# Performance work log

Measured on AMD Instinct MI355X. Metric: run time of the kernel, lower is better.

## Reference

```python
import jax, jax.numpy as jnp
import numpy as np

B, S, HID = 1, 2048, 4096
NH, NKV, D = 32, 8, 128
SCALE = D ** -0.5


def _rope_tables(seq_len, head_dim, base=10000.0):
    inv_freq = 1.0 / (base ** (jnp.arange(0, head_dim, 2, dtype=jnp.float32) / head_dim))
    freqs = jnp.arange(seq_len, dtype=jnp.float32)[:, None] * inv_freq[None, :]  # [S, D/2]
    emb = jnp.concatenate([freqs, freqs], axis=-1)  # [S, D]
    return jnp.cos(emb), jnp.sin(emb)


def _rotate_half(x):
    half = x.shape[-1] // 2
    return jnp.concatenate([-x[..., half:], x[..., :half]], axis=-1)


def setup_inputs() -> dict:
    key = jax.random.key(0)
    ks = jax.random.split(key, 5)
    hidden = jax.random.normal(ks[0], (B, S, HID), dtype=jnp.float32)
    cos, sin = _rope_tables(S, D)
    # additive causal mask: 0 on/below diagonal, large negative above
    neg = jnp.full((S, S), -1e9, dtype=jnp.float32)
    causal_mask = jnp.triu(neg, k=1)[None, None]  # [1,1,S,S]
    std_in = HID ** -0.5
    Wq = jax.random.normal(ks[1], (HID, NH * D), dtype=jnp.float32) * std_in
    Wk = jax.random.normal(ks[2], (HID, NKV * D), dtype=jnp.float32) * std_in
    Wv = jax.random.normal(ks[3], (HID, NKV * D), dtype=jnp.float32) * std_in
    Wo = jax.random.normal(ks[4], (NH * D, HID), dtype=jnp.float32) * ((NH * D) ** -0.5)
    return {"hidden": hidden, "cos": cos, "sin": sin, "causal_mask": causal_mask,
            "Wq": Wq, "Wk": Wk, "Wv": Wv, "Wo": Wo}


def reference(hidden, cos, sin, causal_mask, Wq, Wk, Wv, Wo):
    b, s, _ = hidden.shape
    q = (hidden @ Wq).reshape(b, s, NH, D).transpose(0, 2, 1, 3)    # [B,H,S,D]
    k = (hidden @ Wk).reshape(b, s, NKV, D).transpose(0, 2, 1, 3)   # [B,Hkv,S,D]
    v = (hidden @ Wv).reshape(b, s, NKV, D).transpose(0, 2, 1, 3)
    c = cos[None, None]  # [1,1,S,D]
    sn = sin[None, None]
    q = q * c + _rotate_half(q) * sn
    k = k * c + _rotate_half(k) * sn
    group = NH // NKV
    if group > 1:
        k = jnp.repeat(k, group, axis=1)  # [B,H,S,D]
        v = jnp.repeat(v, group, axis=1)
    scores = jnp.einsum('bhsd,bhtd->bhst', q, k) * SCALE + causal_mask
    attn = jax.nn.softmax(scores.astype(jnp.float32), axis=-1).astype(v.dtype)
    ctx = jnp.einsum('bhst,bhtd->bhsd', attn, v)
    ctx = ctx.transpose(0, 2, 1, 3).reshape(b, s, NH * D)
    return ctx @ Wo
```

## Files before the change

kernel.cpp:

```cpp
#include <hip/hip_runtime.h>
#include <hip/hip_bf16.h>
#include <cstdint>
#include <cstddef>

typedef __attribute__((ext_vector_type(8))) short bf16x8;
typedef __attribute__((ext_vector_type(4))) float f32x4;
typedef __attribute__((ext_vector_type(4))) unsigned int u32x4;

__device__ __forceinline__ unsigned short f2bf(float f) {
  __hip_bfloat16 h = __float2bfloat16(f);
  return *reinterpret_cast<unsigned short*>(&h);
}
__device__ __forceinline__ float bf2f(unsigned short u) {
  __hip_bfloat16 h = *reinterpret_cast<__hip_bfloat16*>(&u);
  return __bfloat162float(h);
}

typedef const __attribute__((address_space(1))) void gas_void;
typedef __attribute__((address_space(3))) void las_void;
__device__ __forceinline__ void gload_lds16(const void* g, void* l) {
  __builtin_amdgcn_global_load_lds((gas_void*)g, (las_void*)l, 16, 0, 0);
}

template <int N>
__device__ __forceinline__ void waitcnt_vm() {
  asm volatile("s_waitcnt vmcnt(%0)" :: "i"(N) : "memory");
}

#define S_LEN 2048
#define HID 4096
#define NH 32
#define NKV 8
#define HD 128
#define NQKV 6144
static const float ATT_SCALE = 0.08838834764831845f;


__global__ void cvt_f32_bf16_kernel(const float* __restrict__ src,
                                    short* __restrict__ dst, int n) {
  int i = (blockIdx.x * 256 + threadIdx.x) * 8;
  if (i >= n) return;
  f32x4 a = *(const f32x4*)(src + i);
  f32x4 b = *(const f32x4*)(src + i + 4);
  unsigned short t[8];
#pragma unroll
  for (int k = 0; k < 4; ++k) { t[k] = f2bf(a[k]); t[4 + k] = f2bf(b[k]); }
  *(u32x4*)(dst + i) = *(const u32x4*)t;
}

__global__ void transpose_cvt_kernel(const float* __restrict__ src,
                                     short* __restrict__ dst, int K, int N) {
  __shared__ float tile[64][33];
  const int kb = blockIdx.x * 64, nb = blockIdx.y * 32;
  const int t = threadIdx.x;
  {
    int kr = t >> 3, c4 = (t & 7) * 4;
#pragma unroll
    for (int i = 0; i < 2; ++i) {
      int k = kr + i * 32;
      f32x4 v = *(const f32x4*)(src + (size_t)(kb + k) * N + nb + c4);
      tile[k][c4] = v[0]; tile[k][c4 + 1] = v[1];
      tile[k][c4 + 2] = v[2]; tile[k][c4 + 3] = v[3];
    }
  }
  __syncthreads();
  int n = t >> 3, k0 = (t & 7) * 8;
  unsigned short o[8];
#pragma unroll
  for (int i = 0; i < 8; ++i) o[i] = f2bf(tile[k0 + i][n]);
  *(u32x4*)(dst + (size_t)(nb + n) * K + kb + k0) = *(const u32x4*)o;
}


#define READ_A(MHL) { \
    const short* As_ = lds + (kt & 1) * BUF; \
    _Pragma("unroll") for (int m = 0; m < MHALF; ++m) \
    _Pragma("unroll") for (int kk = 0; kk < 2; ++kk) { \
      int row = (MHL) * (BM / 2) + wr * MSTEP + m * 16 + r; \
      int c = kk * 4 + g; \
      af[m][kk] = *(const bf16x8*)(As_ + row * 64 + ((c ^ (row & 7)) * 8)); \
    } }
#define READ_B(NHL) { \
    const short* Bs_ = lds + (kt & 1) * BUF + BM * 64; \
    _Pragma("unroll") for (int n = 0; n < NHALF; ++n) \
    _Pragma("unroll") for (int kk = 0; kk < 2; ++kk) { \
      int row = (NHL) * (BN / 2) + wc * NSTEP + n * 16 + r; \
      int c = kk * 4 + g; \
      bf[n][kk] = *(const bf16x8*)(Bs_ + row * 64 + ((c ^ (row & 7)) * 8)); \
    } }
#define MFMA_QUAD(MHL, NHL) { \
    __builtin_amdgcn_s_setprio(1); \
    _Pragma("unroll") for (int m = 0; m < MHALF; ++m) \
    _Pragma("unroll") for (int n = 0; n < NHALF; ++n) \
    _Pragma("unroll") for (int kk = 0; kk < 2; ++kk) \
      acc[(MHL)*MHALF + m][(NHL)*NHALF + n] = __builtin_amdgcn_mfma_f32_16x16x32_bf16( \
          af[m][kk], bf[n][kk], acc[(MHL)*MHALF + m][(NHL)*NHALF + n], 0, 0, 0); \
    __builtin_amdgcn_s_setprio(0); }

template <int MODE, int BM, int BN, int WM, int WN>
__global__ __launch_bounds__(WM * WN * 64, 2) void gemm8p_kernel(
    const short* __restrict__ A, const short* __restrict__ Bt,
    int M, int N, int K,
    float* __restrict__ Cf, short* __restrict__ qb_,
    short* __restrict__ kb_, short* __restrict__ vb_) {
  constexpr int NT = WM * WN * 64;
  constexpr int M_FR = BM / (WM * 16);
  constexpr int N_FR = BN / (WN * 16);
  constexpr int MHALF = M_FR / 2;
  constexpr int NHALF = N_FR / 2;
  constexpr int MSTEP = BM / (2 * WM);
  constexpr int NSTEP = BN / (2 * WN);
  constexpr int LA = (BM / 2) * 8 / NT;
  constexpr int LB = (BN / 2) * 8 / NT;
  constexpr int BUF = (BM + BN) * 64;

  __shared__ short lds[2 * BUF];

  const int tid = threadIdx.x, wid = tid >> 6, lane = tid & 63;
  const int wr = wid / WN, wc = wid % WN;
  const int r = lane & 15, g = lane >> 4;
  const int brow = blockIdx.y * BM, bcol = blockIdx.x * BN;
  const int T = K >> 6;

  f32x4 acc[M_FR][N_FR] = {};
  bf16x8 af[MHALF][2], bf[NHALF][2];

  auto stage_rgn = [&](int kt, int rgn) {
    short* buf = lds + (kt & 1) * BUF;
    if (rgn == 0 || rgn == 3) {
      const int mh = (rgn == 3);
      short* dst = buf + mh * (BM / 2) * 64;
      const short* src = A + (size_t)(brow + mh * (BM / 2)) * K + kt * 64;
#pragma unroll
      for (int i = 0; i < LA; ++i) {
        int slot = i * NT + tid;
        int row = slot >> 3, c2 = slot & 7;
        gload_lds16(src + (size_t)row * K + ((c2 ^ (row & 7)) * 8), dst + slot * 8);
      }
    } else {
      const int nh = (rgn == 2);
      short* dst = buf + BM * 64 + nh * (BN / 2) * 64;
      const short* src = Bt + (size_t)(bcol + nh * (BN / 2)) * K + kt * 64;
#pragma unroll
      for (int i = 0; i < LB; ++i) {
        int slot = i * NT + tid;
        int row = slot >> 3, c2 = slot & 7;
        gload_lds16(src + (size_t)row * K + ((c2 ^ (row & 7)) * 8), dst + slot * 8);
      }
    }
  };

  stage_rgn(0, 0); stage_rgn(0, 1); stage_rgn(0, 2); stage_rgn(0, 3);

  for (int kt = 0; kt < T; ++kt) {
    const bool nl = (kt + 1 < T);
    waitcnt_vm<LA + LB>();
    __builtin_amdgcn_s_barrier();
    __builtin_amdgcn_sched_barrier(0);
    READ_A(0); READ_B(0);
    if (nl) stage_rgn(kt + 1, 0);
    MFMA_QUAD(0, 0);
    if (nl) { waitcnt_vm<2 * LA>(); } else { waitcnt_vm<LA>(); }
    __builtin_amdgcn_s_barrier();
    __builtin_amdgcn_sched_barrier(0);
    READ_B(1);
    if (nl) stage_rgn(kt + 1, 1);
    MFMA_QUAD(0, 1);
    if (nl) { waitcnt_vm<LA + LB>(); } else { waitcnt_vm<0>(); }
    __builtin_amdgcn_s_barrier();
    __builtin_amdgcn_sched_barrier(0);
    READ_A(1);
    if (nl) stage_rgn(kt + 1, 2);
    MFMA_QUAD(1, 1);
    READ_B(0);
    if (nl) stage_rgn(kt + 1, 3);
    MFMA_QUAD(1, 0);
  }

  if (MODE == 0) {
#pragma unroll
    for (int fm = 0; fm < M_FR; ++fm)
#pragma unroll
      for (int fn = 0; fn < N_FR; ++fn)
#pragma unroll
        for (int j = 0; j < 4; ++j) {
          int row = brow + (fm / MHALF) * (BM / 2) + wr * MSTEP + (fm % MHALF) * 16 + g * 4 + j;
          int col = bcol + (fn / NHALF) * (BN / 2) + wc * NSTEP + (fn % NHALF) * 16 + r;
          Cf[(size_t)row * N + col] = acc[fm][fn][j];
        }
  } else {
#pragma unroll
    for (int fn = 0; fn < N_FR; ++fn) {
      const int cb = bcol + (fn / NHALF) * (BN / 2) + wc * NSTEP + (fn % NHALF) * 16;
      if (cb < 4096) {
        unsigned short* dst = (unsigned short*)qb_ + (size_t)(cb >> 7) * S_LEN * HD;
        const int d0 = cb & 127;
#pragma unroll
        for (int fm = 0; fm < M_FR; ++fm)
#pragma unroll
          for (int j = 0; j < 4; ++j) {
            int row = brow + (fm / MHALF) * (BM / 2) + wr * MSTEP + (fm % MHALF) * 16 + g * 4 + j;
            dst[(size_t)row * HD + d0 + r] = f2bf(acc[fm][fn][j]);
          }
      } else if (cb < 5120) {
        char* base = (char*)kb_ + ((size_t)((cb - 4096) >> 7) << 19);
        const int d = (cb & 127) + 0;
#pragma unroll
        for (int fm = 0; fm < M_FR; ++fm)
#pragma unroll
          for (int j = 0; j < 4; ++j) {
            int row = brow + (fm / MHALF) * (BM / 2) + wr * MSTEP + (fm % MHALF) * 16 + g * 4 + j;
            int dd = d + r;
            int krow = row & 63;
            size_t off = ((size_t)(row >> 6) << 14) +
                         ((((krow << 8) + ((dd >> 3) << 4)) ^ ((krow & 7) << 4)) + ((dd & 7) << 1));
            *(unsigned short*)(base + off) = f2bf(acc[fm][fn][j]);
          }
      } else {
        char* base = (char*)vb_ + ((size_t)((cb - 5120) >> 7) << 19);
        const int d = cb & 127;
#pragma unroll
        for (int fm = 0; fm < M_FR; ++fm)
#pragma unroll
          for (int j = 0; j < 4; ++j) {
            int row = brow + (fm / MHALF) * (BM / 2) + wr * MSTEP + (fm % MHALF) * 16 + g * 4 + j;
            int dd = d + r;
            int sl = row & 63;
            size_t off = ((size_t)(row >> 6) << 14) +
                         ((((dd << 7) + ((sl >> 3) << 4)) ^ ((dd & 7) << 4)) + ((sl & 7) << 1));
            *(unsigned short*)(base + off) = f2bf(acc[fm][fn][j]);
          }
      }
    }
  }
}

__global__ void rope_kernel(short* __restrict__ qbuf, short* __restrict__ kbuf,
                            const float* __restrict__ cosT, const float* __restrict__ sinT) {
  int idx = blockIdx.x * 256 + threadIdx.x;
  const int total = (NH + NKV) * S_LEN * 64;
  if (idx >= total) return;
  int d = idx & 63;
  int rowi = idx >> 6;
  int s;
  unsigned short *p1, *p2;
  if (rowi < NH * S_LEN) {
    unsigned short* base = (unsigned short*)qbuf + (size_t)rowi * HD;
    s = rowi & (S_LEN - 1);
    p1 = base + d; p2 = base + d + 64;
  } else {
    int kr = rowi - NH * S_LEN;
    int kvh = kr >> 11; s = kr & (S_LEN - 1);
    char* base = (char*)kbuf + ((size_t)kvh << 19) + ((size_t)(s >> 6) << 14);
    int krow = s & 63, swz = (krow & 7) << 4;
    int dd = d + 64;
    p1 = (unsigned short*)(base + ((((krow << 8) + ((d >> 3) << 4)) ^ swz) + ((d & 7) << 1)));
    p2 = (unsigned short*)(base + ((((krow << 8) + ((dd >> 3) << 4)) ^ swz) + ((dd & 7) << 1)));
  }
  float x1 = bf2f(*p1);
  float x2 = bf2f(*p2);
  float c1 = cosT[s * HD + d], s1 = sinT[s * HD + d];
  *p1 = f2bf(x1 * c1 - x2 * s1);
  *p2 = f2bf(x2 * c1 + x1 * s1);
}

__global__ __launch_bounds__(512, 2) void attn_kernel(const short* __restrict__ qb_,
                                                      const short* __restrict__ kb_,
                                                      const short* __restrict__ vb_,
                                                      short* __restrict__ ctx) {
  const int bid = blockIdx.x;
  const int kvh = bid & 7;
  const int idx = bid >> 3;
  const int h = kvh * 4 + (idx & 3);
  const int slot = idx >> 2;
  const int tid = threadIdx.x, wid = tid >> 6, lane = tid & 63;
  const int r = lane & 15, g = lane >> 4;

  __shared__ short Ks[2][64 * 128];
  __shared__ short Vts[2][128 * 64];
  __shared__ short Ps[8][16 * 64];

  const int qb2s[2] = { slot, 15 - slot };
  const int nt0 = 2 * qb2s[0] + 2;
  const int T = 34;

  const char* kvbase_k = (const char*)kb_ + ((size_t)kvh << 19);
  const char* kvbase_v = (const char*)vb_ + ((size_t)kvh << 19);

  auto stage = [&](int tg, int b) {
    int kvt = (tg < nt0) ? tg : (tg - nt0);
    const char* kt = kvbase_k + ((size_t)kvt << 14);
    const char* vt = kvbase_v + ((size_t)kvt << 14);
#pragma unroll
    for (int i = 0; i < 2; ++i) {
      int ch = i * 8 + wid;
      gload_lds16(kt + ch * 1024 + lane * 16, (char*)&Ks[b][0] + ch * 1024);
      gload_lds16(vt + ch * 1024 + lane * 16, (char*)&Vts[b][0] + ch * 1024);
    }
  };

  stage(0, 0);
  int cur = 0, tglob = 0;

  for (int sec = 0; sec < 2; ++sec) {
    const int qb2 = qb2s[sec];
    const int nt = 2 * qb2 + 2;
    const int rowbase = qb2 * 128 + wid * 16;

    const unsigned short* qptr =
        (const unsigned short*)qb_ + ((size_t)h * S_LEN + rowbase) * HD;
    bf16x8 qf[4];
#pragma unroll
    for (int s4 = 0; s4 < 4; ++s4)
      qf[s4] = *(const bf16x8*)(qptr + (size_t)r * HD + s4 * 32 + g * 8);

    f32x4 oacc[8] = {};
    float m_run[4], l_run[4];
#pragma unroll
    for (int j = 0; j < 4; ++j) { m_run[j] = -1e30f; l_run[j] = 0.f; }

    for (int kvt = 0; kvt < nt; ++kvt, ++tglob) {
      __syncthreads();
      if (tglob + 1 < T) stage(tglob + 1, cur ^ 1);

      const char* Kc = (const char*)&Ks[cur][0];
      const char* Vc = (const char*)&Vts[cur][0];

      f32x4 sv[4] = {};
      __builtin_amdgcn_s_setprio(1);
#pragma unroll
      for (int n = 0; n < 4; ++n) {
        int krow = n * 16 + r;
        int swz = (krow & 7) << 4;
#pragma unroll
        for (int s4 = 0; s4 < 4; ++s4) {
          bf16x8 kf = *(const bf16x8*)(Kc + ((krow * 256 + s4 * 64 + g * 16) ^ swz));
          sv[n] = __builtin_amdgcn_mfma_f32_16x16x32_bf16(qf[s4], kf, sv[n], 0, 0, 0);
        }
      }
      __builtin_amdgcn_s_setprio(0);

      if (kvt * 64 + 63 > rowbase) {
#pragma unroll
        for (int n = 0; n < 4; ++n)
#pragma unroll
          for (int j = 0; j < 4; ++j) {
            int colg = kvt * 64 + n * 16 + r;
            int rowg = rowbase + g * 4 + j;
            sv[n][j] = (colg <= rowg) ? sv[n][j] * ATT_SCALE : -1e30f;
          }
      } else {
#pragma unroll
        for (int n = 0; n < 4; ++n)
#pragma unroll
          for (int j = 0; j < 4; ++j) sv[n][j] *= ATT_SCALE;
      }

      float pmax[4];
#pragma unroll
      for (int j = 0; j < 4; ++j)
        pmax[j] = fmaxf(fmaxf(sv[0][j], sv[1][j]), fmaxf(sv[2][j], sv[3][j]));
#pragma unroll
      for (int msk = 1; msk <= 8; msk <<= 1)
#pragma unroll
        for (int j = 0; j < 4; ++j) pmax[j] = fmaxf(pmax[j], __shfl_xor(pmax[j], msk));

      float sf[4], rsum[4];
#pragma unroll
      for (int j = 0; j < 4; ++j) {
        float mn = fmaxf(m_run[j], pmax[j]);
        sf[j] = __expf(m_run[j] - mn);
        m_run[j] = mn;
        rsum[j] = 0.f;
      }
#pragma unroll
      for (int n = 0; n < 4; ++n)
#pragma unroll
        for (int j = 0; j < 4; ++j) {
          float p = __expf(sv[n][j] - m_run[j]);
          sv[n][j] = p;
          rsum[j] += p;
        }
#pragma unroll
      for (int msk = 1; msk <= 8; msk <<= 1)
#pragma unroll
        for (int j = 0; j < 4; ++j) rsum[j] += __shfl_xor(rsum[j], msk);
#pragma unroll
      for (int j = 0; j < 4; ++j) l_run[j] = l_run[j] * sf[j] + rsum[j];
#pragma unroll
      for (int t = 0; t < 8; ++t)
#pragma unroll
        for (int j = 0; j < 4; ++j) oacc[t][j] *= sf[j];

#pragma unroll
      for (int n = 0; n < 4; ++n)
#pragma unroll
        for (int j = 0; j < 4; ++j) {
          int prow = g * 4 + j, pcol = n * 16 + r;
          int poff = (prow * 128 + pcol * 2) ^ ((prow & 7) << 4);
          *(unsigned short*)((char*)&Ps[wid][0] + poff) = f2bf(sv[n][j]);
        }

      __builtin_amdgcn_s_setprio(1);
#pragma unroll
      for (int s4 = 0; s4 < 2; ++s4) {
        bf16x8 pf = *(const bf16x8*)((const char*)&Ps[wid][0] +
                                     ((r * 128 + s4 * 64 + g * 16) ^ ((r & 7) << 4)));
#pragma unroll
        for (int t = 0; t < 8; ++t) {
          int vrow = t * 16 + r;
          bf16x8 vf = *(const bf16x8*)(Vc + ((vrow * 128 + s4 * 64 + g * 16) ^ ((vrow & 7) << 4)));
          oacc[t] = __builtin_amdgcn_mfma_f32_16x16x32_bf16(pf, vf, oacc[t], 0, 0, 0);
        }
      }
      __builtin_amdgcn_s_setprio(0);
      cur ^= 1;
    }

    float inv[4];
#pragma unroll
    for (int j = 0; j < 4; ++j) inv[j] = 1.0f / l_run[j];
#pragma unroll
    for (int t = 0; t < 8; ++t)
#pragma unroll
      for (int j = 0; j < 4; ++j) {
        int rowg = rowbase + g * 4 + j;
        int colg = h * HD + t * 16 + r;
        ((unsigned short*)ctx)[(size_t)rowg * HID + colg] = f2bf(oacc[t][j] * inv[j]);
      }
  }
}

extern "C" void kernel_launch(void* const* d_in, const int* in_sizes, int n_in,
                              void* d_out, int out_size, void* d_ws, size_t ws_size,
                              hipStream_t stream) {
  const float* hidden = (const float*)d_in[0];
  const float* cosT   = (const float*)d_in[1];
  const float* sinT   = (const float*)d_in[2];
  const float* Wq = (const float*)d_in[4];
  const float* Wk = (const float*)d_in[5];
  const float* Wv = (const float*)d_in[6];
  const float* Wo = (const float*)d_in[7];
  float* out = (float*)d_out;

  char* ws = (char*)d_ws;
  short* hid_bf = (short*)(ws);
  short* Wcat   = (short*)(ws + 16777216);
  short* WoT    = (short*)(ws + 67108864);
  short* qbuf   = (short*)(ws + 100663296);
  short* kbuf   = (short*)(ws + 117440512);
  short* vbuf   = (short*)(ws + 121634816);
  short* ctx    = (short*)(ws + 125829120);

  cvt_f32_bf16_kernel<<<4096, 256, 0, stream>>>(hidden, hid_bf, S_LEN * HID);

  transpose_cvt_kernel<<<dim3(64, 128), 256, 0, stream>>>(Wq, Wcat, HID, 4096);
  transpose_cvt_kernel<<<dim3(64, 32), 256, 0, stream>>>(Wk, Wcat + (size_t)4096 * HID, HID, 1024);
  transpose_cvt_kernel<<<dim3(64, 32), 256, 0, stream>>>(Wv, Wcat + (size_t)5120 * HID, HID, 1024);
  transpose_cvt_kernel<<<dim3(64, 128), 256, 0, stream>>>(Wo, WoT, HID, 4096);

  gemm8p_kernel<1, 256, 256, 2, 4><<<dim3(24, 8), 512, 0, stream>>>(
      hid_bf, Wcat, S_LEN, NQKV, HID, nullptr, qbuf, kbuf, vbuf);

  rope_kernel<<<20480, 256, 0, stream>>>(qbuf, kbuf, cosT, sinT);

  attn_kernel<<<256, 512, 0, stream>>>(qbuf, kbuf, vbuf, ctx);

  gemm8p_kernel<0, 128, 256, 2, 4><<<dim3(16, 16), 512, 0, stream>>>(
      ctx, WoT, S_LEN, HID, HID, out, nullptr, nullptr, nullptr);
}
```

Before: 339.1 us.

## Restructure GEMM k-loop into barrier-separated phases with double B-fragment registers

The GEMM main loop is reorganised into phases. In each phase, LDS fragment reads and the next tile's global-to-LDS loads are issued, then a barrier and an lgkmcnt(0) wait run before a high-priority MFMA block. B fragments are held in two register sets, so the last quad no longer re-reads B half 0 from LDS. The output projection tile shape also changes from 128x256 to 256x128 with a 4x2 wave layout. The aim is to align waves for ping-pong scheduling and cut redundant LDS reads, at the cost of extra barriers and more fragment registers.

```diff
diff --git a/kernel.cpp b/kernel.cpp
--- a/kernel.cpp
+++ b/kernel.cpp
@@ -26,6 +26,8 @@
 __device__ __forceinline__ void waitcnt_vm() {
   asm volatile("s_waitcnt vmcnt(%0)" :: "i"(N) : "memory");
 }
+#define LGKM0 { asm volatile("s_waitcnt lgkmcnt(0)" ::: "memory"); \
+                __builtin_amdgcn_sched_barrier(0); }
 
 #define S_LEN 2048
 #define HID 4096
@@ -80,22 +82,20 @@
       int c = kk * 4 + g; \
       af[m][kk] = *(const bf16x8*)(As_ + row * 64 + ((c ^ (row & 7)) * 8)); \
     } }
-#define READ_B(NHL) { \
+#define READ_B(NHL, ARR) { \
     const short* Bs_ = lds + (kt & 1) * BUF + BM * 64; \
     _Pragma("unroll") for (int n = 0; n < NHALF; ++n) \
     _Pragma("unroll") for (int kk = 0; kk < 2; ++kk) { \
       int row = (NHL) * (BN / 2) + wc * NSTEP + n * 16 + r; \
       int c = kk * 4 + g; \
-      bf[n][kk] = *(const bf16x8*)(Bs_ + row * 64 + ((c ^ (row & 7)) * 8)); \
+      ARR[n][kk] = *(const bf16x8*)(Bs_ + row * 64 + ((c ^ (row & 7)) * 8)); \
     } }
-#define MFMA_QUAD(MHL, NHL) { \
-    __builtin_amdgcn_s_setprio(1); \
+#define MFMA_QUAD(MHL, NHL, ARR) { \
     _Pragma("unroll") for (int m = 0; m < MHALF; ++m) \
     _Pragma("unroll") for (int n = 0; n < NHALF; ++n) \
     _Pragma("unroll") for (int kk = 0; kk < 2; ++kk) \
       acc[(MHL)*MHALF + m][(NHL)*NHALF + n] = __builtin_amdgcn_mfma_f32_16x16x32_bf16( \
-          af[m][kk], bf[n][kk], acc[(MHL)*MHALF + m][(NHL)*NHALF + n], 0, 0, 0); \
-    __builtin_amdgcn_s_setprio(0); }
+          af[m][kk], ARR[n][kk], acc[(MHL)*MHALF + m][(NHL)*NHALF + n], 0, 0, 0); }
 
 template <int MODE, int BM, int BN, int WM, int WN>
 __global__ __launch_bounds__(WM * WN * 64, 2) void gemm8p_kernel(
@@ -123,7 +123,7 @@
   const int T = K >> 6;
 
   f32x4 acc[M_FR][N_FR] = {};
-  bf16x8 af[MHALF][2], bf[NHALF][2];
+  bf16x8 af[MHALF][2], bf0[NHALF][2], bf1[NHALF][2];
 
   auto stage_rgn = [&](int kt, int rgn) {
     short* buf = lds + (kt & 1) * BUF;
@@ -151,30 +151,42 @@
   };
 
   stage_rgn(0, 0); stage_rgn(0, 1); stage_rgn(0, 2); stage_rgn(0, 3);
+  waitcnt_vm<LA + LB>();
+  __builtin_amdgcn_s_barrier();
 
   for (int kt = 0; kt < T; ++kt) {
     const bool nl = (kt + 1 < T);
-    waitcnt_vm<LA + LB>();
-    __builtin_amdgcn_s_barrier();
+    READ_A(0); READ_B(0, bf0);
+    if (nl) stage_rgn(kt + 1, 0);
     __builtin_amdgcn_sched_barrier(0);
-    READ_A(0); READ_B(0);
-    if (nl) stage_rgn(kt + 1, 0);
-    MFMA_QUAD(0, 0);
+    __builtin_amdgcn_s_barrier();
+    LGKM0;
+    __builtin_amdgcn_s_setprio(1);
+    MFMA_QUAD(0, 0, bf0);
+    __builtin_amdgcn_s_setprio(0);
     if (nl) { waitcnt_vm<2 * LA>(); } else { waitcnt_vm<LA>(); }
     __builtin_amdgcn_s_barrier();
+    READ_B(1, bf1);
+    if (nl) stage_rgn(kt + 1, 1);
     __builtin_amdgcn_sched_barrier(0);
-    READ_B(1);
-    if (nl) stage_rgn(kt + 1, 1);
-    MFMA_QUAD(0, 1);
+    __builtin_amdgcn_s_barrier();
+    LGKM0;
+    __builtin_amdgcn_s_setprio(1);
+    MFMA_QUAD(0, 1, bf1);
+    __builtin_amdgcn_s_setprio(0);
     if (nl) { waitcnt_vm<LA + LB>(); } else { waitcnt_vm<0>(); }
     __builtin_amdgcn_s_barrier();
+    READ_A(1);
+    if (nl) { stage_rgn(kt + 1, 2); stage_rgn(kt + 1, 3); }
     __builtin_amdgcn_sched_barrier(0);
-    READ_A(1);
-    if (nl) stage_rgn(kt + 1, 2);
-    MFMA_QUAD(1, 1);
-    READ_B(0);
-    if (nl) stage_rgn(kt + 1, 3);
-    MFMA_QUAD(1, 0);
+    __builtin_amdgcn_s_barrier();
+    LGKM0;
+    __builtin_amdgcn_s_setprio(1);
+    MFMA_QUAD(1, 1, bf1);
+    MFMA_QUAD(1, 0, bf0);
+    __builtin_amdgcn_s_setprio(0);
+    if (nl) { waitcnt_vm<LA + LB>(); }
+    __builtin_amdgcn_s_barrier();
   }
 
   if (MODE == 0) {
@@ -204,7 +216,7 @@
           }
       } else if (cb < 5120) {
         char* base = (char*)kb_ + ((size_t)((cb - 4096) >> 7) << 19);
-        const int d = (cb & 127) + 0;
+        const int d = cb & 127;
 #pragma unroll
         for (int fm = 0; fm < M_FR; ++fm)
 #pragma unroll
@@ -466,6 +478,6 @@
 
   attn_kernel<<<256, 512, 0, stream>>>(qbuf, kbuf, vbuf, ctx);
 
-  gemm8p_kernel<0, 128, 256, 2, 4><<<dim3(16, 16), 512, 0, stream>>>(
+  gemm8p_kernel<0, 256, 128, 4, 2><<<dim3(32, 8), 512, 0, stream>>>(
       ctx, WoT, S_LEN, HID, HID, out, nullptr, nullptr, nullptr);
 }
```

Result: slower. 355.4 us (+4.8%).
